# Optimization experiments

Hardware: AMD Instinct MI355X
Metric: run time of the kernel (lower is better)

## Reference

```python
import jax, jax.numpy as jnp
import numpy as np

B, H, S, DH = 2, 16, 2048, 64
MASK_FILL = -10000.0


def setup_inputs() -> dict:
    key = jax.random.key(0)
    kq, kk, kv = jax.random.split(key, 3)
    q = jax.random.normal(kq, (B, H, S, DH), dtype=jnp.float32)
    k = jax.random.normal(kk, (B, H, S, DH), dtype=jnp.float32)
    v = jax.random.normal(kv, (B, H, S, DH), dtype=jnp.float32)
    # causal mask: True where attention is disallowed (upper triangle)
    mask = jnp.triu(jnp.ones((S, S), dtype=jnp.bool_), k=1)
    return {"q": q, "k": k, "v": v, "mask": mask}


def reference(q, k, v, mask):
    scale = 1.0 / jnp.sqrt(jnp.asarray(k.shape[-1], dtype=q.dtype))
    # scores: [B, H, S_q, S_k]
    scores = jnp.einsum("bhqd,bhkd->bhqk", q, k) * scale
    # additive mask: masked_fill on a zeros [S_k, S_v] matrix -> -10000 where mask
    attn_bias = jnp.where(mask, jnp.asarray(MASK_FILL, dtype=k.dtype),
                          jnp.asarray(0.0, dtype=k.dtype))
    scores = scores + attn_bias  # broadcast over batch/heads
    attn = jax.nn.softmax(scores, axis=-1)
    # dropout_rate = 0.0 -> identity
    return jnp.einsum("bhqk,bhkd->bhqd", attn, v)
```

## Files before the change

kernel.cpp:

```cpp
#include <hip/hip_runtime.h>


#define S_LEN  2048
#define DHDIM  64
#define NHEADS 32
#define LDP    72
#define M2     23.083120654223414f
#define QSCALE 0.18033688011117658f

typedef __attribute__((ext_vector_type(8))) short bf16x8;
typedef __attribute__((ext_vector_type(4))) float f32x4;

__device__ __constant__ unsigned char T_QT[48] = {
    31,31,30,15, 30,29,29,28,14, 28,27,27,26,13, 26,25,25,24,12,
    24,23,23,22,11, 22,21,21,20,10, 20,19,19,18,9, 18,17,17,16,8,
    16,7, 6,5,4,3,2,1,0};
__device__ __constant__ unsigned char T_K0[48] = {
    0,16,0,0, 16,0,15,0,0, 15,0,14,0,0, 14,0,13,0,0,
    13,0,12,0,0, 12,0,11,0,0, 11,0,10,0,0, 10,0,9,0,0,
    9,0, 0,0,0,0,0,0,0};
__device__ __constant__ unsigned char T_K1[48] = {
    16,32,16,16, 31,15,30,15,15, 29,14,28,14,14, 27,13,26,13,13,
    25,12,24,12,12, 23,11,22,11,11, 21,10,20,10,10, 19,9,18,9,9,
    17,8, 7,6,5,4,3,2,1};

__device__ __forceinline__ float fast_exp2(float x) {
#if __has_builtin(__builtin_amdgcn_exp2f)
    return __builtin_amdgcn_exp2f(x);
#else
    return exp2f(x);
#endif
}
__device__ __forceinline__ unsigned short f2bf(float f) {
    unsigned u = __float_as_uint(f);
    return (unsigned short)((u + 0x7fffu + ((u >> 16) & 1u)) >> 16);
}
__device__ __forceinline__ void ld8(const float* p, float* f) {
    float4 a = *(const float4*)p, b = *(const float4*)(p + 4);
    f[0]=a.x; f[1]=a.y; f[2]=a.z; f[3]=a.w; f[4]=b.x; f[5]=b.y; f[6]=b.z; f[7]=b.w;
}
__device__ __forceinline__ uint4 pack8(const float* f, float scale) {
    union { uint4 v; unsigned short s[8]; } w;
    #pragma unroll
    for (int j = 0; j < 8; j++) w.s[j] = f2bf(f[j] * scale);
    return w.v;
}
__device__ __forceinline__ unsigned packhi(float a, float b) {
#if __has_builtin(__builtin_amdgcn_perm)
    return __builtin_amdgcn_perm(__float_as_uint(b), __float_as_uint(a), 0x07060302u);
#else
    return (__float_as_uint(a) >> 16) | (__float_as_uint(b) & 0xffff0000u);
#endif
}
__device__ __forceinline__ bf16x8 pad4(unsigned lo, unsigned hi) {
    union { unsigned u[4]; bf16x8 v; } w;
    w.u[0] = lo; w.u[1] = hi; w.u[2] = 0u; w.u[3] = 0u;
    return w.v;
}

__global__ __launch_bounds__(256) void prep(
    const float* __restrict__ Qf, const float* __restrict__ Kf,
    const float* __restrict__ Vf, unsigned short* __restrict__ qb,
    unsigned short* __restrict__ kb, unsigned short* __restrict__ vtb)
{
    const int st = blockIdx.x, bh = blockIdx.y;
    __shared__ unsigned lt32[64][LDP / 2];
    const float* vp = Vf + ((size_t)bh * S_LEN + st * 64) * DHDIM;
    {
        const int c = threadIdx.x;
        const int sp = c >> 3;
        const int d0 = (c & 7) * 8;
        float fa[8], fb[8];
        ld8(vp + (2 * sp) * DHDIM + d0, fa);
        ld8(vp + (2 * sp + 1) * DHDIM + d0, fb);
        #pragma unroll
        for (int j = 0; j < 8; j++) {
            int d = d0 + j;
            int colw = (sp & 3) | ((((sp >> 2) ^ (d >> 3)) & 7) << 2);
            lt32[d][colw] = (unsigned)f2bf(fa[j]) | ((unsigned)f2bf(fb[j]) << 16);
        }
    }
    size_t off = ((size_t)(bh * 32 + st) * 4096) + (size_t)threadIdx.x * 16;
    float f[8];
    ld8(Qf + off, f);     *(uint4*)(qb + off)     = pack8(f, QSCALE);
    ld8(Qf + off + 8, f); *(uint4*)(qb + off + 8) = pack8(f, QSCALE);
    ld8(Kf + off, f);     *(uint4*)(kb + off)     = pack8(f, 1.0f);
    ld8(Kf + off + 8, f); *(uint4*)(kb + off + 8) = pack8(f, 1.0f);
    __syncthreads();
    unsigned short* op = vtb + (size_t)bh * DHDIM * S_LEN + st * 64;
    for (int c = threadIdx.x; c < 512; c += 256) {
        int d = c >> 3, q = c & 7;
        int colw = ((q ^ (d >> 3)) & 7) << 2;
        *(uint4*)(op + (size_t)d * S_LEN + q * 8) = *(const uint4*)&lt32[d][colw];
    }
}

__global__ __launch_bounds__(512, 4) void fattn_splitk(
    const unsigned short* __restrict__ Qp, const unsigned short* __restrict__ Kp,
    const unsigned short* __restrict__ Vp,
    float* __restrict__ pO, float* __restrict__ pL, float* __restrict__ O)
{
    __shared__ unsigned short smem[320 * LDP];
    unsigned short (*ksA)[LDP] = (unsigned short(*)[LDP])smem;
    unsigned short (*ksB)[LDP] = (unsigned short(*)[LDP])(smem + 64 * LDP);
    unsigned short (*vtA)[LDP] = (unsigned short(*)[LDP])(smem + 128 * LDP);
    unsigned short (*vtB)[LDP] = (unsigned short(*)[LDP])(smem + 192 * LDP);
    unsigned short (*qs)[LDP]  = (unsigned short(*)[LDP])(smem + 256 * LDP);

    const int bh   = blockIdx.x;
    const int rank = blockIdx.y;
    const int qt   = T_QT[rank];
    const int k0   = T_K0[rank];
    const int k1   = T_K1[rank];
    const bool whole = (k1 - k0 == qt + 1);

    const int tid  = threadIdx.x;
    const int wave = tid >> 6, lane = tid & 63;
    const int quad = lane >> 4, l16 = lane & 15;
    const int kslice = wave & 3, qhalf = wave >> 2;

    {
        const unsigned short* src = Qp + ((size_t)bh * S_LEN + qt * 64) * DHDIM;
        int row = tid >> 3, c8 = (tid & 7) * 8;
        *(uint4*)&qs[row][c8] = *(const uint4*)(src + row * DHDIM + c8);
    }
    __syncthreads();
    const bf16x8 bq00 = *(const bf16x8*)&qs[qhalf * 32 + l16][quad * 8];
    const bf16x8 bq01 = *(const bf16x8*)&qs[qhalf * 32 + l16][32 + quad * 8];
    const bf16x8 bq10 = *(const bf16x8*)&qs[qhalf * 32 + 16 + l16][quad * 8];
    const bf16x8 bq11 = *(const bf16x8*)&qs[qhalf * 32 + 16 + l16][32 + quad * 8];

    bf16x8 ones8;
    #pragma unroll
    for (int j = 0; j < 8; j++) ones8[j] = (j < 4) ? (short)0x3F80 : (short)0;

    f32x4 of[4][2];
    #pragma unroll
    for (int dg = 0; dg < 4; dg++) {
        of[dg][0] = (f32x4){0.f, 0.f, 0.f, 0.f};
        of[dg][1] = (f32x4){0.f, 0.f, 0.f, 0.f};
    }
    f32x4 ofl0 = (f32x4){0.f, 0.f, 0.f, 0.f};
    f32x4 ofl1 = (f32x4){0.f, 0.f, 0.f, 0.f};

    const unsigned short* Kbh = Kp + (size_t)bh * S_LEN * DHDIM;
    const unsigned short* Vbh = Vp + (size_t)bh * DHDIM * S_LEN;
    const int sr = tid >> 3, sc = (tid & 7) * 8;
    uint4 kr, vr;
    kr = *(const uint4*)(Kbh + ((size_t)k0 * 64 + sr) * DHDIM + sc);
    vr = *(const uint4*)(Vbh + (size_t)sr * S_LEN + k0 * 64 + sc);
    {
        unsigned short (*ks)[LDP] = (k0 & 1) ? ksB : ksA;
        unsigned short (*vt)[LDP] = (k0 & 1) ? vtB : vtA;
        *(uint4*)&ks[sr][sc] = kr;
        *(uint4*)&vt[sr][sc] = vr;
    }
    if (k0 + 1 < k1) {
        kr = *(const uint4*)(Kbh + ((size_t)(k0 + 1) * 64 + sr) * DHDIM + sc);
        vr = *(const uint4*)(Vbh + (size_t)sr * S_LEN + (k0 + 1) * 64 + sc);
    }

    for (int kt = k0; kt < k1; kt++) {
        __syncthreads();

        if (kt + 1 < k1) {
            unsigned short (*ks)[LDP] = ((kt + 1) & 1) ? ksB : ksA;
            unsigned short (*vt)[LDP] = ((kt + 1) & 1) ? vtB : vtA;
            *(uint4*)&ks[sr][sc] = kr;
            *(uint4*)&vt[sr][sc] = vr;
            if (kt + 2 < k1) {
                kr = *(const uint4*)(Kbh + ((size_t)(kt + 2) * 64 + sr) * DHDIM + sc);
                vr = *(const uint4*)(Vbh + (size_t)sr * S_LEN + (kt + 2) * 64 + sc);
            }
        }
        const unsigned short (*ksc)[LDP] = (kt & 1) ? ksB : ksA;
        const unsigned short (*vtc)[LDP] = (kt & 1) ? vtB : vtA;

        const bf16x8 ak0 = *(const bf16x8*)&ksc[kslice * 16 + l16][quad * 8];
        const bf16x8 ak1 = *(const bf16x8*)&ksc[kslice * 16 + l16][32 + quad * 8];
        f32x4 sf0 = (f32x4){-M2, -M2, -M2, -M2};
        f32x4 sf1 = (f32x4){-M2, -M2, -M2, -M2};
        sf0 = __builtin_amdgcn_mfma_f32_16x16x32_bf16(ak0, bq00, sf0, 0, 0, 0);
        sf0 = __builtin_amdgcn_mfma_f32_16x16x32_bf16(ak1, bq01, sf0, 0, 0, 0);
        sf1 = __builtin_amdgcn_mfma_f32_16x16x32_bf16(ak0, bq10, sf1, 0, 0, 0);
        sf1 = __builtin_amdgcn_mfma_f32_16x16x32_bf16(ak1, bq11, sf1, 0, 0, 0);

        const bool diag = (kt == qt);
        float p0[4], p1[4];
        #pragma unroll
        for (int r = 0; r < 4; r++) {
            p0[r] = fast_exp2(sf0[r]);
            p1[r] = fast_exp2(sf1[r]);
            if (diag) {
                const int kloc = kslice * 16 + quad * 4 + r;
                if (kloc > qhalf * 32 + l16)      p0[r] = 0.f;
                if (kloc > qhalf * 32 + 16 + l16) p1[r] = 0.f;
            }
        }
        const bf16x8 bp0 = pad4(packhi(p0[0], p0[1]), packhi(p0[2], p0[3]));
        const bf16x8 bp1 = pad4(packhi(p1[0], p1[1]), packhi(p1[2], p1[3]));
        ofl0 = __builtin_amdgcn_mfma_f32_16x16x32_bf16(ones8, bp0, ofl0, 0, 0, 0);
        ofl1 = __builtin_amdgcn_mfma_f32_16x16x32_bf16(ones8, bp1, ofl1, 0, 0, 0);

        #pragma unroll
        for (int dg = 0; dg < 4; dg++) {
            const unsigned* vp32 =
                (const unsigned*)&vtc[dg * 16 + l16][kslice * 16 + quad * 4];
            const bf16x8 av = pad4(vp32[0], vp32[1]);
            of[dg][0] = __builtin_amdgcn_mfma_f32_16x16x32_bf16(av, bp0, of[dg][0], 0, 0, 0);
            of[dg][1] = __builtin_amdgcn_mfma_f32_16x16x32_bf16(av, bp1, of[dg][1], 0, 0, 0);
        }
    }

    __syncthreads();
    float* fs = (float*)smem;
    const int rb = lane * 18;
    #pragma unroll
    for (int pass = 0; pass < 2; pass++) {
        const int d0 = pass * 2;
        if (kslice >= 2) {
            float* w = fs + (qhalf * 2 + (kslice - 2)) * (64 * 18) + rb;
            #pragma unroll
            for (int d = 0; d < 2; d++)
                #pragma unroll
                for (int n2 = 0; n2 < 2; n2++)
                    #pragma unroll
                    for (int r = 0; r < 4; r++)
                        w[d * 8 + n2 * 4 + r] = of[d0 + d][n2][r];
            if (pass) { w[16] = ofl0[0]; w[17] = ofl1[0]; }
        }
        __syncthreads();
        if (kslice < 2) {
            const float* rd = fs + (qhalf * 2 + kslice) * (64 * 18) + rb;
            #pragma unroll
            for (int d = 0; d < 2; d++)
                #pragma unroll
                for (int n2 = 0; n2 < 2; n2++)
                    #pragma unroll
                    for (int r = 0; r < 4; r++)
                        of[d0 + d][n2][r] += rd[d * 8 + n2 * 4 + r];
            if (pass) { ofl0[0] += rd[16]; ofl1[0] += rd[17]; }
        }
        __syncthreads();
        if (kslice == 1) {
            float* w = fs + qhalf * (64 * 18) + rb;
            #pragma unroll
            for (int d = 0; d < 2; d++)
                #pragma unroll
                for (int n2 = 0; n2 < 2; n2++)
                    #pragma unroll
                    for (int r = 0; r < 4; r++)
                        w[d * 8 + n2 * 4 + r] = of[d0 + d][n2][r];
            if (pass) { w[16] = ofl0[0]; w[17] = ofl1[0]; }
        }
        __syncthreads();
        if (kslice == 0) {
            const float* rd = fs + qhalf * (64 * 18) + rb;
            #pragma unroll
            for (int d = 0; d < 2; d++)
                #pragma unroll
                for (int n2 = 0; n2 < 2; n2++)
                    #pragma unroll
                    for (int r = 0; r < 4; r++)
                        of[d0 + d][n2][r] += rd[d * 8 + n2 * 4 + r];
            if (pass) { ofl0[0] += rd[16]; ofl1[0] += rd[17]; }
        }
        __syncthreads();
    }

    if (kslice == 0) {
        const int q0 = qt * 64 + qhalf * 32 + l16;
        const int q1 = q0 + 16;
        if (whole) {
            const float inv0 = 1.f / ofl0[0];
            const float inv1 = 1.f / ofl1[0];
            float* o0 = O + ((size_t)bh * S_LEN + q0) * DHDIM;
            float* o1 = O + ((size_t)bh * S_LEN + q1) * DHDIM;
            #pragma unroll
            for (int dg = 0; dg < 4; dg++) {
                *(float4*)(o0 + dg * 16 + quad * 4) = make_float4(
                    of[dg][0][0] * inv0, of[dg][0][1] * inv0,
                    of[dg][0][2] * inv0, of[dg][0][3] * inv0);
                *(float4*)(o1 + dg * 16 + quad * 4) = make_float4(
                    of[dg][1][0] * inv1, of[dg][1][1] * inv1,
                    of[dg][1][2] * inv1, of[dg][1][3] * inv1);
            }
        } else {
            const int slot = ((bh * 16 + (qt - 16)) << 1) | (k0 != 0 ? 1 : 0);
            const int r0 = qhalf * 32 + l16, r1 = r0 + 16;
            if (quad == 0) {
                pL[slot * 64 + r0] = ofl0[0];
                pL[slot * 64 + r1] = ofl1[0];
            }
            float* p0p = pO + (size_t)slot * 4096 + r0 * 64;
            float* p1p = pO + (size_t)slot * 4096 + r1 * 64;
            #pragma unroll
            for (int dg = 0; dg < 4; dg++) {
                *(float4*)(p0p + dg * 16 + quad * 4) = make_float4(
                    of[dg][0][0], of[dg][0][1], of[dg][0][2], of[dg][0][3]);
                *(float4*)(p1p + dg * 16 + quad * 4) = make_float4(
                    of[dg][1][0], of[dg][1][1], of[dg][1][2], of[dg][1][3]);
            }
        }
    }
}

__global__ __launch_bounds__(256) void combine(
    const float* __restrict__ pO, const float* __restrict__ pL,
    float* __restrict__ O)
{
    const int qt = 16 + blockIdx.x, bh = blockIdx.y;
    const int sa = ((bh * 16 + (qt - 16)) << 1), sb = sa | 1;
    const float* A = pO + (size_t)sa * 4096;
    const float* B = pO + (size_t)sb * 4096;
    float* out = O + ((size_t)bh * S_LEN + qt * 64) * DHDIM;
    #pragma unroll
    for (int k = 0; k < 4; k++) {
        int c = threadIdx.x + k * 256;
        int row = c >> 4;
        float inv = 1.f / (pL[sa * 64 + row] + pL[sb * 64 + row]);
        float4 a = *(const float4*)(A + c * 4);
        float4 b = *(const float4*)(B + c * 4);
        *(float4*)(out + c * 4) = make_float4(
            (a.x + b.x) * inv, (a.y + b.y) * inv,
            (a.z + b.z) * inv, (a.w + b.w) * inv);
    }
}

template <bool PRE>
__global__ __launch_bounds__(256) void fattn_kernel(
    const void* __restrict__ Qp, const void* __restrict__ Kp,
    const void* __restrict__ Vp, float* __restrict__ O)
{
    __shared__ unsigned short smem[192 * LDP];
    unsigned short (*ks)[LDP]  = (unsigned short(*)[LDP])smem;
    unsigned short (*vts)[LDP] = (unsigned short(*)[LDP])(smem + 64 * LDP);
    unsigned short (*qs)[LDP]  = (unsigned short(*)[LDP])(smem + 128 * LDP);
    unsigned short (*pst)[LDP] = qs;

    const int id = blockIdx.y * 32 + blockIdx.x;
    const int g  = id >> 8;
    const int r8 = id & 255;
    const int bh = r8 >> 3;
    const int s8 = r8 & 7;
    const int qt = (g == 0) ? 31 - 2 * s8 : (g == 1) ? 2 * s8
                 : (g == 2) ? 30 - 2 * s8 : 2 * s8 + 1;

    const int tid = threadIdx.x;
    const int wave = tid >> 6, lane = tid & 63;
    const int quad = lane >> 4, l16 = lane & 15;

    if constexpr (PRE) {
        const unsigned short* src = (const unsigned short*)Qp
            + ((size_t)bh * S_LEN + qt * 64) * DHDIM;
        for (int c = tid; c < 512; c += 256) {
            int row = c >> 3, c8 = (c & 7) * 8;
            *(uint4*)&qs[row][c8] = *(const uint4*)(src + row * DHDIM + c8);
        }
    } else {
        const float* src = (const float*)Qp + ((size_t)bh * S_LEN + qt * 64) * DHDIM;
        for (int c = tid; c < 512; c += 256) {
            int row = c >> 3, c8 = (c & 7) * 8;
            float f[8]; ld8(src + row * DHDIM + c8, f);
            *(uint4*)&qs[row][c8] = pack8(f, QSCALE);
        }
    }
    __syncthreads();

    const int prow = wave * 16 + l16;
    const bf16x8 bq0 = *(const bf16x8*)&qs[prow][quad * 8];
    const bf16x8 bq1 = *(const bf16x8*)&qs[prow][32 + quad * 8];

    float l_p = 0.f;
    f32x4 of[4];
    #pragma unroll
    for (int n = 0; n < 4; n++) of[n] = (f32x4){0.f, 0.f, 0.f, 0.f};

    for (int kt = 0; kt <= qt; kt++) {
        __syncthreads();
        if constexpr (PRE) {
            const unsigned short* ksrc = (const unsigned short*)Kp
                + ((size_t)bh * S_LEN + kt * 64) * DHDIM;
            const unsigned short* vsrc = (const unsigned short*)Vp
                + (size_t)bh * DHDIM * S_LEN + kt * 64;
            for (int c = tid; c < 512; c += 256) {
                int row = c >> 3, c8 = (c & 7) * 8;
                *(uint4*)&ks[row][c8]  = *(const uint4*)(ksrc + row * DHDIM + c8);
                *(uint4*)&vts[row][c8] = *(const uint4*)(vsrc + (size_t)row * S_LEN + c8);
            }
        } else {
            const float* ksrc = (const float*)Kp + ((size_t)bh * S_LEN + kt * 64) * DHDIM;
            const float* vsrc = (const float*)Vp + ((size_t)bh * S_LEN + kt * 64) * DHDIM;
            for (int c = tid; c < 512; c += 256) {
                int row = c >> 3, c8 = (c & 7) * 8;
                float f[8];
                ld8(ksrc + row * DHDIM + c8, f);
                *(uint4*)&ks[row][c8] = pack8(f, 1.0f);
                ld8(vsrc + row * DHDIM + c8, f);
                #pragma unroll
                for (int j = 0; j < 8; j++) vts[c8 + j][row] = f2bf(f[j]);
            }
        }
        __syncthreads();

        f32x4 sf[4];
        #pragma unroll
        for (int n = 0; n < 4; n++) {
            bf16x8 ak0 = *(const bf16x8*)&ks[n * 16 + l16][quad * 8];
            bf16x8 ak1 = *(const bf16x8*)&ks[n * 16 + l16][32 + quad * 8];
            sf[n] = (f32x4){-M2, -M2, -M2, -M2};
            sf[n] = __builtin_amdgcn_mfma_f32_16x16x32_bf16(ak0, bq0, sf[n], 0, 0, 0);
            sf[n] = __builtin_amdgcn_mfma_f32_16x16x32_bf16(ak1, bq1, sf[n], 0, 0, 0);
        }

        const bool diag = (kt == qt);
        #pragma unroll
        for (int n = 0; n < 4; n++) {
            float p[4];
            #pragma unroll
            for (int r = 0; r < 4; r++) {
                p[r] = fast_exp2(sf[n][r]);
                if (diag && (n * 16 + quad * 4 + r > prow)) p[r] = 0.f;
                l_p += p[r];
            }
            uint2 dw;
            dw.x = packhi(p[0], p[1]);
            dw.y = packhi(p[2], p[3]);
            *(uint2*)&pst[prow][n * 16 + quad * 4] = dw;
        }
        asm volatile("s_waitcnt lgkmcnt(0)" ::: "memory");

        bf16x8 bp0 = *(const bf16x8*)&pst[prow][quad * 8];
        bf16x8 bp1 = *(const bf16x8*)&pst[prow][32 + quad * 8];
        #pragma unroll
        for (int n = 0; n < 4; n++) {
            bf16x8 av0 = *(const bf16x8*)&vts[n * 16 + l16][quad * 8];
            bf16x8 av1 = *(const bf16x8*)&vts[n * 16 + l16][32 + quad * 8];
            of[n] = __builtin_amdgcn_mfma_f32_16x16x32_bf16(av0, bp0, of[n], 0, 0, 0);
            of[n] = __builtin_amdgcn_mfma_f32_16x16x32_bf16(av1, bp1, of[n], 0, 0, 0);
        }
    }

    l_p += __shfl_xor(l_p, 16);
    l_p += __shfl_xor(l_p, 32);
    const float inv = 1.f / l_p;
    float* op = O + ((size_t)bh * S_LEN + qt * 64 + prow) * DHDIM;
    #pragma unroll
    for (int n = 0; n < 4; n++)
        *(float4*)(op + n * 16 + quad * 4) = make_float4(
            of[n][0] * inv, of[n][1] * inv, of[n][2] * inv, of[n][3] * inv);
}

extern "C" void kernel_launch(void* const* d_in, const int* in_sizes, int n_in,
                              void* d_out, int out_size, void* d_ws, size_t ws_size,
                              hipStream_t stream) {
    const float* Q = (const float*)d_in[0];
    const float* K = (const float*)d_in[1];
    const float* V = (const float*)d_in[2];
    float* O = (float*)d_out;
    const size_t N = (size_t)NHEADS * S_LEN * DHDIM;
    const size_t prepB  = 3 * N * sizeof(unsigned short);
    const size_t partB  = (size_t)1024 * (4096 + 64) * sizeof(float);

    if (d_ws && ws_size >= prepB + partB) {
        unsigned short* qb  = (unsigned short*)d_ws;
        unsigned short* kb  = qb + N;
        unsigned short* vtb = kb + N;
        float* pO = (float*)((char*)d_ws + prepB);
        float* pL = pO + (size_t)1024 * 4096;
        prep<<<dim3(S_LEN / 64, NHEADS), 256, 0, stream>>>(Q, K, V, qb, kb, vtb);
        fattn_splitk<<<dim3(32, 48), 512, 0, stream>>>(qb, kb, vtb, pO, pL, O);
        combine<<<dim3(16, 32), 256, 0, stream>>>(pO, pL, O);
    } else if (d_ws && ws_size >= prepB) {
        unsigned short* qb  = (unsigned short*)d_ws;
        unsigned short* kb  = qb + N;
        unsigned short* vtb = kb + N;
        prep<<<dim3(S_LEN / 64, NHEADS), 256, 0, stream>>>(Q, K, V, qb, kb, vtb);
        fattn_kernel<true><<<dim3(32, 32), 256, 0, stream>>>(qb, kb, vtb, O);
    } else {
        fattn_kernel<false><<<dim3(32, 32), 256, 0, stream>>>(Q, K, V, O);
    }
}
```

Before: 143.7 us.

## Load K and V fragments directly from global into registers, drop LDS staging

The attention kernel stops staging K and V tiles through double-buffered shared memory. Each lane now loads its own MFMA operand fragments straight from global memory into registers, prefetching one tile ahead, which removes the per-iteration barrier and the LDS writes and reads. Shared memory shrinks to a buffer reused for Q and the final reduction, which could raise occupancy. The trade-off is that each wave issues uncoalesced, partly redundant global loads (the V rows come as 8-byte pieces) and relies on L2/L1 caching instead of block-wide reuse, and there is less latency hiding per wave.

```diff
diff --git a/kernel.cpp b/kernel.cpp
--- a/kernel.cpp
+++ b/kernel.cpp
@@ -56,6 +56,9 @@
     union { unsigned u[4]; bf16x8 v; } w;
     w.u[0] = lo; w.u[1] = hi; w.u[2] = 0u; w.u[3] = 0u;
     return w.v;
+}
+__device__ __forceinline__ bf16x8 as_bf16x8(uint4 v) {
+    union { uint4 u; bf16x8 b; } w; w.u = v; return w.b;
 }
 
 __global__ __launch_bounds__(256) void prep(
@@ -100,12 +103,8 @@
     const unsigned short* __restrict__ Vp,
     float* __restrict__ pO, float* __restrict__ pL, float* __restrict__ O)
 {
-    __shared__ unsigned short smem[320 * LDP];
-    unsigned short (*ksA)[LDP] = (unsigned short(*)[LDP])smem;
-    unsigned short (*ksB)[LDP] = (unsigned short(*)[LDP])(smem + 64 * LDP);
-    unsigned short (*vtA)[LDP] = (unsigned short(*)[LDP])(smem + 128 * LDP);
-    unsigned short (*vtB)[LDP] = (unsigned short(*)[LDP])(smem + 192 * LDP);
-    unsigned short (*qs)[LDP]  = (unsigned short(*)[LDP])(smem + 256 * LDP);
+    __shared__ float fs[4608];
+    unsigned short (*qs)[LDP] = (unsigned short(*)[LDP])fs;
 
     const int bh   = blockIdx.x;
     const int rank = blockIdx.y;
@@ -129,6 +128,7 @@
     const bf16x8 bq01 = *(const bf16x8*)&qs[qhalf * 32 + l16][32 + quad * 8];
     const bf16x8 bq10 = *(const bf16x8*)&qs[qhalf * 32 + 16 + l16][quad * 8];
     const bf16x8 bq11 = *(const bf16x8*)&qs[qhalf * 32 + 16 + l16][32 + quad * 8];
+    __syncthreads();
 
     bf16x8 ones8;
     #pragma unroll
@@ -143,41 +143,39 @@
     f32x4 ofl0 = (f32x4){0.f, 0.f, 0.f, 0.f};
     f32x4 ofl1 = (f32x4){0.f, 0.f, 0.f, 0.f};
 
-    const unsigned short* Kbh = Kp + (size_t)bh * S_LEN * DHDIM;
-    const unsigned short* Vbh = Vp + (size_t)bh * DHDIM * S_LEN;
-    const int sr = tid >> 3, sc = (tid & 7) * 8;
-    uint4 kr, vr;
-    kr = *(const uint4*)(Kbh + ((size_t)k0 * 64 + sr) * DHDIM + sc);
-    vr = *(const uint4*)(Vbh + (size_t)sr * S_LEN + k0 * 64 + sc);
+    const unsigned short* kbase = Kp + (size_t)bh * S_LEN * DHDIM
+        + (size_t)(kslice * 16 + l16) * DHDIM + quad * 8;
+    const unsigned short* vbase = Vp + (size_t)bh * DHDIM * S_LEN
+        + (size_t)l16 * S_LEN + kslice * 16 + quad * 4;
+
+    uint4 kr0, kr1; uint2 vr0, vr1, vr2, vr3;
     {
-        unsigned short (*ks)[LDP] = (k0 & 1) ? ksB : ksA;
-        unsigned short (*vt)[LDP] = (k0 & 1) ? vtB : vtA;
-        *(uint4*)&ks[sr][sc] = kr;
-        *(uint4*)&vt[sr][sc] = vr;
-    }
-    if (k0 + 1 < k1) {
-        kr = *(const uint4*)(Kbh + ((size_t)(k0 + 1) * 64 + sr) * DHDIM + sc);
-        vr = *(const uint4*)(Vbh + (size_t)sr * S_LEN + (k0 + 1) * 64 + sc);
+        const unsigned short* kp = kbase + (size_t)k0 * (64 * DHDIM);
+        const unsigned short* vp = vbase + k0 * 64;
+        kr0 = *(const uint4*)(kp);
+        kr1 = *(const uint4*)(kp + 32);
+        vr0 = *(const uint2*)(vp);
+        vr1 = *(const uint2*)(vp + 16 * S_LEN);
+        vr2 = *(const uint2*)(vp + 32 * S_LEN);
+        vr3 = *(const uint2*)(vp + 48 * S_LEN);
     }
 
     for (int kt = k0; kt < k1; kt++) {
-        __syncthreads();
+        const bf16x8 ak0 = as_bf16x8(kr0);
+        const bf16x8 ak1 = as_bf16x8(kr1);
+        const uint2 cv0 = vr0, cv1 = vr1, cv2 = vr2, cv3 = vr3;
 
         if (kt + 1 < k1) {
-            unsigned short (*ks)[LDP] = ((kt + 1) & 1) ? ksB : ksA;
-            unsigned short (*vt)[LDP] = ((kt + 1) & 1) ? vtB : vtA;
-            *(uint4*)&ks[sr][sc] = kr;
-            *(uint4*)&vt[sr][sc] = vr;
-            if (kt + 2 < k1) {
-                kr = *(const uint4*)(Kbh + ((size_t)(kt + 2) * 64 + sr) * DHDIM + sc);
-                vr = *(const uint4*)(Vbh + (size_t)sr * S_LEN + (kt + 2) * 64 + sc);
-            }
-        }
-        const unsigned short (*ksc)[LDP] = (kt & 1) ? ksB : ksA;
-        const unsigned short (*vtc)[LDP] = (kt & 1) ? vtB : vtA;
-
-        const bf16x8 ak0 = *(const bf16x8*)&ksc[kslice * 16 + l16][quad * 8];
-        const bf16x8 ak1 = *(const bf16x8*)&ksc[kslice * 16 + l16][32 + quad * 8];
+            const unsigned short* kp = kbase + (size_t)(kt + 1) * (64 * DHDIM);
+            const unsigned short* vp = vbase + (kt + 1) * 64;
+            kr0 = *(const uint4*)(kp);
+            kr1 = *(const uint4*)(kp + 32);
+            vr0 = *(const uint2*)(vp);
+            vr1 = *(const uint2*)(vp + 16 * S_LEN);
+            vr2 = *(const uint2*)(vp + 32 * S_LEN);
+            vr3 = *(const uint2*)(vp + 48 * S_LEN);
+        }
+
         f32x4 sf0 = (f32x4){-M2, -M2, -M2, -M2};
         f32x4 sf1 = (f32x4){-M2, -M2, -M2, -M2};
         sf0 = __builtin_amdgcn_mfma_f32_16x16x32_bf16(ak0, bq00, sf0, 0, 0, 0);
@@ -202,18 +200,23 @@
         ofl0 = __builtin_amdgcn_mfma_f32_16x16x32_bf16(ones8, bp0, ofl0, 0, 0, 0);
         ofl1 = __builtin_amdgcn_mfma_f32_16x16x32_bf16(ones8, bp1, ofl1, 0, 0, 0);
 
-        #pragma unroll
-        for (int dg = 0; dg < 4; dg++) {
-            const unsigned* vp32 =
-                (const unsigned*)&vtc[dg * 16 + l16][kslice * 16 + quad * 4];
-            const bf16x8 av = pad4(vp32[0], vp32[1]);
-            of[dg][0] = __builtin_amdgcn_mfma_f32_16x16x32_bf16(av, bp0, of[dg][0], 0, 0, 0);
-            of[dg][1] = __builtin_amdgcn_mfma_f32_16x16x32_bf16(av, bp1, of[dg][1], 0, 0, 0);
+        {
+            const bf16x8 av0 = pad4(cv0.x, cv0.y);
+            of[0][0] = __builtin_amdgcn_mfma_f32_16x16x32_bf16(av0, bp0, of[0][0], 0, 0, 0);
+            of[0][1] = __builtin_amdgcn_mfma_f32_16x16x32_bf16(av0, bp1, of[0][1], 0, 0, 0);
+            const bf16x8 av1 = pad4(cv1.x, cv1.y);
+            of[1][0] = __builtin_amdgcn_mfma_f32_16x16x32_bf16(av1, bp0, of[1][0], 0, 0, 0);
+            of[1][1] = __builtin_amdgcn_mfma_f32_16x16x32_bf16(av1, bp1, of[1][1], 0, 0, 0);
+            const bf16x8 av2 = pad4(cv2.x, cv2.y);
+            of[2][0] = __builtin_amdgcn_mfma_f32_16x16x32_bf16(av2, bp0, of[2][0], 0, 0, 0);
+            of[2][1] = __builtin_amdgcn_mfma_f32_16x16x32_bf16(av2, bp1, of[2][1], 0, 0, 0);
+            const bf16x8 av3 = pad4(cv3.x, cv3.y);
+            of[3][0] = __builtin_amdgcn_mfma_f32_16x16x32_bf16(av3, bp0, of[3][0], 0, 0, 0);
+            of[3][1] = __builtin_amdgcn_mfma_f32_16x16x32_bf16(av3, bp1, of[3][1], 0, 0, 0);
         }
     }
 
     __syncthreads();
-    float* fs = (float*)smem;
     const int rb = lane * 18;
     #pragma unroll
     for (int pass = 0; pass < 2; pass++) {
```

Result: slower. 204.4 us (+42.3%).
